# Kernel tuning notes

Hardware: AMD Instinct MI355X
Metric: run time of the kernel (lower is better)

Reference implementation:

```python
import math
import jax, jax.numpy as jnp
import numpy as np

NUM_BUCKETS = 32
MAX_DISTANCE = 128
N_HEADS = 16
D_KV = 64


def _relative_position_bucket(relative_position, num_buckets=NUM_BUCKETS, max_distance=MAX_DISTANCE):
    # bidirectional variant (encoder): half the buckets for each sign
    nb = num_buckets // 2
    n = -relative_position
    ret = (n < 0).astype(jnp.int32) * nb
    n = jnp.abs(n)
    max_exact = nb // 2
    is_small = n < max_exact
    val_if_large = max_exact + (
        jnp.log(jnp.maximum(n, 1).astype(jnp.float32) / max_exact)
        / math.log(max_distance / max_exact)
        * (nb - max_exact)
    ).astype(jnp.int32)
    val_if_large = jnp.minimum(val_if_large, nb - 1)
    return ret + jnp.where(is_small, n, val_if_large)


def setup_inputs() -> dict:
    key = jax.random.key(0)
    ks = jax.random.split(key, 6)
    d_model = 1024
    inner = N_HEADS * D_KV
    scale = 1.0 / math.sqrt(d_model)
    x = jax.random.normal(ks[0], (2, 2048, d_model), dtype=jnp.float32)
    wq = jax.random.normal(ks[1], (d_model, inner), dtype=jnp.float32) * scale
    wk = jax.random.normal(ks[2], (d_model, inner), dtype=jnp.float32) * scale
    wv = jax.random.normal(ks[3], (d_model, inner), dtype=jnp.float32) * scale
    wo = jax.random.normal(ks[4], (inner, d_model), dtype=jnp.float32) * scale
    rel_emb = jax.random.normal(ks[5], (NUM_BUCKETS, N_HEADS), dtype=jnp.float32)
    return {"x": x, "wq": wq, "wk": wk, "wv": wv, "wo": wo, "rel_emb": rel_emb}


def reference(x, wq, wk, wv, wo, rel_emb):
    B, S, D = x.shape
    # QKV projections (no bias, T5 style), split heads -> [B, S, H, Dk]
    q = (x @ wq).reshape(B, S, N_HEADS, D_KV)
    k = (x @ wk).reshape(B, S, N_HEADS, D_KV)
    v = (x @ wv).reshape(B, S, N_HEADS, D_KV)
    # NOTE: T5 does NOT scale by 1/sqrt(d_kv)
    scores = jnp.einsum("bqhd,bkhd->bhqk", q, k)  # [B, H, S, S]
    # relative position bias
    ctx = jnp.arange(S)[:, None]
    mem = jnp.arange(S)[None, :]
    buckets = _relative_position_bucket(mem - ctx)  # [S, S]
    bias = rel_emb[buckets]  # [S, S, H]
    bias = jnp.transpose(bias, (2, 0, 1))[None]  # [1, H, S, S]
    scores = scores + bias
    weights = jax.nn.softmax(scores.astype(jnp.float32), axis=-1).astype(scores.dtype)
    context = jnp.einsum("bhqk,bkhd->bqhd", weights, v).reshape(B, S, N_HEADS * D_KV)
    return context @ wo
```

## Files before the change

kernel.cpp:

```cpp
#include <hip/hip_runtime.h>
#include <hip/hip_bf16.h>

typedef __attribute__((ext_vector_type(8))) _Float16 f16x8;
typedef __attribute__((ext_vector_type(4))) float f32x4;
typedef unsigned short u16;
typedef unsigned int u32;

#define S_LEN 2048
#define NH    16
#define DK    64
#define DMODEL 1024
#define LSTR  40
#define LOG2E 1.44269504f
#define NTILES (S_LEN / 64)

union F16U { _Float16 h; u16 u; };
__device__ __forceinline__ u16 f2h(float f) {
    F16U v; v.h = (_Float16)f; return v.u;
}

__device__ __forceinline__ void gl16(const u16* g, u16* l) {
    __builtin_amdgcn_global_load_lds(
        (__attribute__((address_space(1))) void*)(u16*)g,
        (__attribute__((address_space(3))) void*)l, 16, 0, 0);
}

__global__ __launch_bounds__(256) void bias_table_kernel(
    const float* __restrict__ rel_emb, float* __restrict__ tab)
{
    int idx = blockIdx.x * 256 + threadIdx.x;
    int h = idx >> 12;
    int t = idx & 4095;
    int rp = t - 2048;
    int n = -rp;
    int ret = 0;
    if (n < 0) { ret = 16; n = -n; }
    int inner;
    if (n < 8) {
        inner = n;
    } else {
        inner = 8 + (n >= 12) + (n >= 16) + (n >= 23) + (n >= 32)
                  + (n >= 46) + (n >= 64) + (n >= 91);
        if (inner > 15) inner = 15;
    }
    tab[h * 4096 + t] = rel_emb[(ret + inner) * NH + h] * LOG2E;
}

__global__ __launch_bounds__(256) void convert_x(
    const float* __restrict__ X, u16* __restrict__ Xf)
{
    long i8 = ((long)blockIdx.x * 256 + threadIdx.x) * 8;
    float4 a = *(const float4*)&X[i8];
    float4 b = *(const float4*)&X[i8 + 4];
    *(ushort4*)&Xf[i8] =
        make_ushort4(f2h(a.x), f2h(a.y), f2h(a.z), f2h(a.w));
    *(ushort4*)&Xf[i8 + 4] =
        make_ushort4(f2h(b.x), f2h(b.y), f2h(b.z), f2h(b.w));
}

__global__ __launch_bounds__(256) void convert_wT(
    const float* __restrict__ Wq, const float* __restrict__ Wk,
    const float* __restrict__ Wv, const float* __restrict__ Wo,
    u16* __restrict__ WT)
{
    const float* src = (blockIdx.z == 0) ? Wq : (blockIdx.z == 1) ? Wk
                     : (blockIdx.z == 2) ? Wv : Wo;
    u16* dT = WT + (long)blockIdx.z * 1048576;
    __shared__ __align__(16) float T[64 * 68];
    const int k0 = blockIdx.y * 64, n0 = blockIdx.x * 64;
    const int tid = threadIdx.x;
    #pragma unroll
    for (int u = 0; u < 4; u++) {
        int w = tid + u * 256;
        int r = w >> 4, c4 = (w & 15) * 4;
        *(float4*)&T[r * 68 + c4] =
            *(const float4*)&src[(long)(k0 + r) * DMODEL + n0 + c4];
    }
    __syncthreads();
    #pragma unroll
    for (int u = 0; u < 4; u++) {
        int w = tid + u * 256;
        int n = w >> 4, kc = (w & 15) * 4;
        *(ushort4*)&dT[(long)(n0 + n) * DMODEL + k0 + kc] = make_ushort4(
            f2h(T[(kc + 0) * 68 + n]), f2h(T[(kc + 1) * 68 + n]),
            f2h(T[(kc + 2) * 68 + n]), f2h(T[(kc + 3) * 68 + n]));
    }
}

__global__ __launch_bounds__(256, 3) void gemm_qkv_mfma(
    const u16* __restrict__ Xf, const u16* __restrict__ WT,
    u16* __restrict__ Qf, u16* __restrict__ Kf, u16* __restrict__ VT)
{
    const int z = blockIdx.z;
    const u16* BT = WT + (long)z * 1048576;

    __shared__ __align__(16) u16 Ah[128 * LSTR], Bh[128 * LSTR];

    const int tid = threadIdx.x;
    const int wv = tid >> 6, lane = tid & 63;
    const int g = lane >> 4, li = lane & 15;
    const int wr = wv >> 1, wc = wv & 1;
    const int bm = blockIdx.y * 128, bn = blockIdx.x * 128;

    const int srow = tid >> 2, sq8 = (tid & 3) * 8;
    const u16* As0 = &Xf[(long)(bm + srow) * DMODEL + sq8];
    const u16* As1 = As0 + 64 * DMODEL;
    const u16* Bs0 = &BT[(long)(bn + srow) * DMODEL + sq8];
    const u16* Bs1 = Bs0 + 64 * DMODEL;
    u16* AL0 = &Ah[srow * LSTR + sq8];
    u16* AL1 = &Ah[(srow + 64) * LSTR + sq8];
    u16* BL0 = &Bh[srow * LSTR + sq8];
    u16* BL1 = &Bh[(srow + 64) * LSTR + sq8];

    f32x4 acc[4][4];
    #pragma unroll
    for (int i = 0; i < 4; i++)
        #pragma unroll
        for (int j = 0; j < 4; j++) acc[i][j] = (f32x4){0.f, 0.f, 0.f, 0.f};

    *(uint4*)AL0 = *(const uint4*)As0;
    *(uint4*)AL1 = *(const uint4*)As1;
    *(uint4*)BL0 = *(const uint4*)Bs0;
    *(uint4*)BL1 = *(const uint4*)Bs1;
    __syncthreads();

    for (int k0 = 0; k0 < DMODEL; k0 += 32) {
        const bool have = (k0 + 32) < DMODEL;
        uint4 na0, na1, nb0, nb1;
        if (have) {
            na0 = *(const uint4*)(As0 + k0 + 32);
            na1 = *(const uint4*)(As1 + k0 + 32);
            nb0 = *(const uint4*)(Bs0 + k0 + 32);
            nb1 = *(const uint4*)(Bs1 + k0 + 32);
        }

        f16x8 a_h[4], b_h[4];
        #pragma unroll
        for (int i = 0; i < 4; i++)
            a_h[i] = *(const f16x8*)&Ah[(wr * 64 + i * 16 + li) * LSTR + g * 8];
        #pragma unroll
        for (int j = 0; j < 4; j++)
            b_h[j] = *(const f16x8*)&Bh[(wc * 64 + j * 16 + li) * LSTR + g * 8];
        #pragma unroll
        for (int i = 0; i < 4; i++)
            #pragma unroll
            for (int j = 0; j < 4; j++)
                acc[i][j] = __builtin_amdgcn_mfma_f32_16x16x32_f16(
                    a_h[i], b_h[j], acc[i][j], 0, 0, 0);

        if (have) {
            __syncthreads();
            *(uint4*)AL0 = na0; *(uint4*)AL1 = na1;
            *(uint4*)BL0 = nb0; *(uint4*)BL1 = nb1;
            __syncthreads();
        }
    }

    if (z == 2) {
        #pragma unroll
        for (int i = 0; i < 4; i++) {
            int s_base = bm + wr * 64 + i * 16 + g * 4;
            int bb = s_base >> 11, s = s_base & 2047;
            #pragma unroll
            for (int j = 0; j < 4; j++) {
                int gcol = bn + wc * 64 + j * 16 + li;
                int hh = gcol >> 6, d = gcol & 63;
                long idx = (((long)(bb * NH + hh)) * DK + d) * S_LEN + s;
                *(ushort4*)&VT[idx] = make_ushort4(
                    f2h(acc[i][j][0]), f2h(acc[i][j][1]),
                    f2h(acc[i][j][2]), f2h(acc[i][j][3]));
            }
        }
    } else {
        u16* O = (z == 0) ? Qf : Kf;
        #pragma unroll
        for (int i = 0; i < 4; i++) {
            #pragma unroll
            for (int r = 0; r < 4; r++) {
                int grow = bm + wr * 64 + i * 16 + g * 4 + r;
                int bb = grow >> 11, s = grow & 2047;
                #pragma unroll
                for (int j = 0; j < 4; j++) {
                    int gcol = bn + wc * 64 + j * 16 + li;
                    int hh = gcol >> 6, d = gcol & 63;
                    long idx = (((long)(bb * NH + hh)) * S_LEN + s) * DK + d;
                    O[idx] = f2h(acc[i][j][r]);
                }
            }
        }
    }
}

__global__ __launch_bounds__(256, 3) void gemm_out_mfma(
    const u16* __restrict__ Ab, const u16* __restrict__ WT,
    float* __restrict__ O)
{
    const u16* BT = WT + 3L * 1048576;
    __shared__ __align__(16) u16 Ah[128 * LSTR], Bh[128 * LSTR];

    const int tid = threadIdx.x;
    const int wv = tid >> 6, lane = tid & 63;
    const int g = lane >> 4, li = lane & 15;
    const int wr = wv >> 1, wc = wv & 1;
    const int bm = blockIdx.y * 128, bn = blockIdx.x * 128;

    const int srow = tid >> 2, sq8 = (tid & 3) * 8;
    const u16* As0 = &Ab[(long)(bm + srow) * DMODEL + sq8];
    const u16* As1 = As0 + 64 * DMODEL;
    const u16* Bs0 = &BT[(long)(bn + srow) * DMODEL + sq8];
    const u16* Bs1 = Bs0 + 64 * DMODEL;
    u16* AL0 = &Ah[srow * LSTR + sq8];
    u16* AL1 = &Ah[(srow + 64) * LSTR + sq8];
    u16* BL0 = &Bh[srow * LSTR + sq8];
    u16* BL1 = &Bh[(srow + 64) * LSTR + sq8];

    f32x4 acc[4][4];
    #pragma unroll
    for (int i = 0; i < 4; i++)
        #pragma unroll
        for (int j = 0; j < 4; j++) acc[i][j] = (f32x4){0.f, 0.f, 0.f, 0.f};

    *(uint4*)AL0 = *(const uint4*)As0;
    *(uint4*)AL1 = *(const uint4*)As1;
    *(uint4*)BL0 = *(const uint4*)Bs0;
    *(uint4*)BL1 = *(const uint4*)Bs1;
    __syncthreads();

    for (int k0 = 0; k0 < DMODEL; k0 += 32) {
        const bool have = (k0 + 32) < DMODEL;
        uint4 na0, na1, nb0, nb1;
        if (have) {
            na0 = *(const uint4*)(As0 + k0 + 32);
            na1 = *(const uint4*)(As1 + k0 + 32);
            nb0 = *(const uint4*)(Bs0 + k0 + 32);
            nb1 = *(const uint4*)(Bs1 + k0 + 32);
        }

        f16x8 a_h[4], b_h[4];
        #pragma unroll
        for (int i = 0; i < 4; i++)
            a_h[i] = *(const f16x8*)&Ah[(wr * 64 + i * 16 + li) * LSTR + g * 8];
        #pragma unroll
        for (int j = 0; j < 4; j++)
            b_h[j] = *(const f16x8*)&Bh[(wc * 64 + j * 16 + li) * LSTR + g * 8];
        #pragma unroll
        for (int i = 0; i < 4; i++)
            #pragma unroll
            for (int j = 0; j < 4; j++)
                acc[i][j] = __builtin_amdgcn_mfma_f32_16x16x32_f16(
                    a_h[i], b_h[j], acc[i][j], 0, 0, 0);

        if (have) {
            __syncthreads();
            *(uint4*)AL0 = na0; *(uint4*)AL1 = na1;
            *(uint4*)BL0 = nb0; *(uint4*)BL1 = nb1;
            __syncthreads();
        }
    }

    #pragma unroll
    for (int i = 0; i < 4; i++)
        #pragma unroll
        for (int r = 0; r < 4; r++) {
            int grow = bm + wr * 64 + i * 16 + g * 4 + r;
            #pragma unroll
            for (int j = 0; j < 4; j++) {
                int gcol = bn + wc * 64 + j * 16 + li;
                O[(long)grow * DMODEL + gcol] = acc[i][j][r];
            }
        }
}

__global__ __launch_bounds__(256, 4) void attn_mfma(
    const u16* __restrict__ Qf, const u16* __restrict__ Kf,
    const u16* __restrict__ VT, const float* __restrict__ tab,
    u16* __restrict__ ctxb)
{
    __shared__ __align__(16) u16 Ks[2][4096];
    __shared__ __align__(16) u16 Vs[2][4096];

    const int tid = threadIdx.x;
    const int wv = tid >> 6, lane = tid & 63;
    const int g = lane >> 4, li = lane & 15;

    const int nbid = (blockIdx.x & 7) * 128 + (blockIdx.x >> 3);
    const int qblk = nbid & 31;
    const int h = (nbid >> 5) & 15;
    const int b = nbid >> 9;
    const int q0 = qblk * 64;
    const long bh = b * NH + h;
    const int qloc = wv * 16 + li;

    const u16* KhG = Kf + bh * (S_LEN * DK);
    const u16* VtG = VT + bh * (DK * S_LEN);
    const float* th0 = tab + h * 4096;
    const float* thq = th0 + 2048 - q0 - qloc + g * 4;

    const int sr  = lane >> 3;
    const int sd8 = ((lane & 7) ^ sr) * 8;
    const int c0 = wv * 2, c1 = wv * 2 + 1;
    const u16* Kg0 = KhG + (long)(c0 * 8 + sr) * DK + sd8;
    const u16* Kg1 = KhG + (long)(c1 * 8 + sr) * DK + sd8;
    const u16* Vg0 = VtG + (long)(c0 * 8 + sr) * S_LEN + sd8;
    const u16* Vg1 = VtG + (long)(c1 * 8 + sr) * S_LEN + sd8;

    const int sw  = (li & 7) * 8;
    const int roA = (g * 8) ^ sw;
    const int roB = (g * 8 + 32) ^ sw;
    const int rrow = li * 64;

    f16x8 q0f, q1f;
    {
        long qrow = bh * S_LEN + q0 + qloc;
        const u16* ph = Qf + qrow * DK + g * 8;
        q0f = *(const f16x8*)ph;  q1f = *(const f16x8*)(ph + 32);
    }
    const float bias_hi = th0[2048 + 512];
    const float bias_lo = th0[2048 - 512];

    gl16(Kg0, &Ks[0][c0 * 512]);
    gl16(Kg1, &Ks[0][c1 * 512]);
    gl16(Vg0, &Vs[0][c0 * 512]);
    gl16(Vg1, &Vs[0][c1 * 512]);
    __syncthreads();

    f32x4 Oc[4];
    #pragma unroll
    for (int n = 0; n < 4; n++) Oc[n] = (f32x4){0.f, 0.f, 0.f, 0.f};
    float mP = -1e30f, lR = 0.f;

    int cur = 0;
    for (int t = 0; t < NTILES; ++t) {
        const int kt0 = t * 64;

        if (t + 1 < NTILES) {
            const long ko = (long)(kt0 + 64) * DK;
            gl16(Kg0 + ko, &Ks[cur ^ 1][c0 * 512]);
            gl16(Kg1 + ko, &Ks[cur ^ 1][c1 * 512]);
            gl16(Vg0 + kt0 + 64, &Vs[cur ^ 1][c0 * 512]);
            gl16(Vg1 + kt0 + 64, &Vs[cur ^ 1][c1 * 512]);
        }

        float bia[4][4];
        const int dd = kt0 - q0;
        if (dd >= 192 || dd <= -192) {
            const float bc = (dd > 0) ? bias_hi : bias_lo;
            #pragma unroll
            for (int m = 0; m < 4; m++)
                #pragma unroll
                for (int r = 0; r < 4; r++) bia[m][r] = bc;
        } else {
            const float* tb = thq + kt0;
            #pragma unroll
            for (int m = 0; m < 4; m++)
                #pragma unroll
                for (int r = 0; r < 4; r++) bia[m][r] = tb[m * 16 + r];
        }

        f32x4 Sa[4];
        __builtin_amdgcn_s_setprio(1);
        #pragma unroll
        for (int m = 0; m < 4; m++) {
            const u16* kp = &Ks[cur][m * 1024 + rrow];
            f16x8 k0 = *(const f16x8*)(kp + roA);
            f16x8 k1 = *(const f16x8*)(kp + roB);
            f32x4 s = (f32x4){0.f, 0.f, 0.f, 0.f};
            s = __builtin_amdgcn_mfma_f32_16x16x32_f16(k0, q0f, s, 0, 0, 0);
            s = __builtin_amdgcn_mfma_f32_16x16x32_f16(k1, q1f, s, 0, 0, 0);
            Sa[m] = s;
        }
        __builtin_amdgcn_s_setprio(0);

        #pragma unroll
        for (int m = 0; m < 4; m++)
            #pragma unroll
            for (int r = 0; r < 4; r++)
                Sa[m][r] = fmaf(Sa[m][r], LOG2E, bia[m][r]);

        float mm[4];
        #pragma unroll
        for (int m = 0; m < 4; m++)
            mm[m] = fmaxf(fmaxf(Sa[m][0], Sa[m][1]),
                          fmaxf(Sa[m][2], Sa[m][3]));
        float pm = fmaxf(fmaxf(mm[0], mm[1]), fmaxf(mm[2], mm[3]));
        pm = fmaxf(pm, __shfl_xor(pm, 16));
        pm = fmaxf(pm, __shfl_xor(pm, 32));

        if (__any(pm > mP)) {
            float mn = fmaxf(mP, pm);
            float alpha = __builtin_amdgcn_exp2f(mP - mn);
            mP = mn;
            lR *= alpha;
            float aO[4];
            #pragma unroll
            for (int r = 0; r < 4; r++) aO[r] = __shfl(alpha, g * 4 + r);
            #pragma unroll
            for (int n = 0; n < 4; n++)
                #pragma unroll
                for (int r = 0; r < 4; r++) Oc[n][r] *= aO[r];
        }

        float sm[4];
        #pragma unroll
        for (int m = 0; m < 4; m++) {
            #pragma unroll
            for (int r = 0; r < 4; r++)
                Sa[m][r] = __builtin_amdgcn_exp2f(Sa[m][r] - mP);
            sm[m] = (Sa[m][0] + Sa[m][1]) + (Sa[m][2] + Sa[m][3]);
        }
        float ls = (sm[0] + sm[1]) + (sm[2] + sm[3]);
        ls += __shfl_xor(ls, 16);
        ls += __shfl_xor(ls, 32);
        lR += ls;

        u32 y0, y1, y2, y3, y4, y5, y6, y7;
        {
            y0 = f2h(Sa[0][0]) | ((u32)f2h(Sa[0][1]) << 16);
            y1 = f2h(Sa[0][2]) | ((u32)f2h(Sa[0][3]) << 16);
            y2 = f2h(Sa[1][0]) | ((u32)f2h(Sa[1][1]) << 16);
            y3 = f2h(Sa[1][2]) | ((u32)f2h(Sa[1][3]) << 16);
            y4 = f2h(Sa[2][0]) | ((u32)f2h(Sa[2][1]) << 16);
            y5 = f2h(Sa[2][2]) | ((u32)f2h(Sa[2][3]) << 16);
            y6 = f2h(Sa[3][0]) | ((u32)f2h(Sa[3][1]) << 16);
            y7 = f2h(Sa[3][2]) | ((u32)f2h(Sa[3][3]) << 16);
        }
        {
            bool hi = (lane & 32) != 0;
            u32 s0 = hi ? y0 : y2, s1 = hi ? y1 : y3;
            u32 s4 = hi ? y4 : y6, s5 = hi ? y5 : y7;
            u32 r0 = __shfl_xor((int)s0, 32);
            u32 r1 = __shfl_xor((int)s1, 32);
            u32 r4 = __shfl_xor((int)s4, 32);
            u32 r5 = __shfl_xor((int)s5, 32);
            if (hi) { y0 = r0; y1 = r1; y4 = r4; y5 = r5; }
            else    { y2 = r0; y3 = r1; y6 = r4; y7 = r5; }
        }
        {
            bool hi = (lane & 16) != 0;
            u32 s0 = hi ? y0 : y2, s1 = hi ? y1 : y3;
            u32 s4 = hi ? y4 : y6, s5 = hi ? y5 : y7;
            u32 r0 = __shfl_xor((int)s0, 16);
            u32 r1 = __shfl_xor((int)s1, 16);
            u32 r4 = __shfl_xor((int)s4, 16);
            u32 r5 = __shfl_xor((int)s5, 16);
            if (hi) { y0 = r0; y1 = r1; y4 = r4; y5 = r5; }
            else    { y2 = r0; y3 = r1; y6 = r4; y7 = r5; }
        }
        union { uint4 u; f16x8 h; } P0, P1;
        P0.u = make_uint4(y0, y1, y2, y3);
        P1.u = make_uint4(y4, y5, y6, y7);

        __builtin_amdgcn_s_setprio(1);
        #pragma unroll
        for (int n = 0; n < 4; n++) {
            const u16* vp = &Vs[cur][n * 1024 + rrow];
            f16x8 v0 = *(const f16x8*)(vp + roA);
            f16x8 v1 = *(const f16x8*)(vp + roB);
            Oc[n] = __builtin_amdgcn_mfma_f32_16x16x32_f16(P0.h, v0, Oc[n], 0, 0, 0);
            Oc[n] = __builtin_amdgcn_mfma_f32_16x16x32_f16(P1.h, v1, Oc[n], 0, 0, 0);
        }
        __builtin_amdgcn_s_setprio(0);

        __syncthreads();
        cur ^= 1;
    }

    float linv = 1.0f / lR;
    float iv[4];
    #pragma unroll
    for (int r = 0; r < 4; r++) iv[r] = __shfl(linv, g * 4 + r);
    #pragma unroll
    for (int n = 0; n < 4; n++)
        #pragma unroll
        for (int r = 0; r < 4; r++)
            ctxb[((long)(b * S_LEN + q0 + wv * 16 + g * 4 + r)) * DMODEL
                 + h * DK + n * 16 + li] = f2h(Oc[n][r] * iv[r]);
}

extern "C" void kernel_launch(void* const* d_in, const int* in_sizes, int n_in,
                              void* d_out, int out_size, void* d_ws, size_t ws_size,
                              hipStream_t stream)
{
    const float* x    = (const float*)d_in[0];
    const float* wq   = (const float*)d_in[1];
    const float* wk   = (const float*)d_in[2];
    const float* wv   = (const float*)d_in[3];
    const float* wo   = (const float*)d_in[4];
    const float* rel  = (const float*)d_in[5];

    u16* W0 = (u16*)d_ws;
    u16* Xf  = W0;
    u16* Qf  = W0 + 4194304;
    u16* Kf  = W0 + 8388608;
    u16* VT  = W0 + 12582912;
    u16* WT  = W0 + 16777216;
    float* tab = (float*)(W0 + 20971520);
    u16* ctxb = Xf;

    bias_table_kernel<<<dim3(256), dim3(256), 0, stream>>>(rel, tab);
    convert_x<<<dim3(2048), dim3(256), 0, stream>>>(x, Xf);
    convert_wT<<<dim3(16, 16, 4), dim3(256), 0, stream>>>(wq, wk, wv, wo, WT);
    gemm_qkv_mfma<<<dim3(8, 32, 3), dim3(256), 0, stream>>>(Xf, WT, Qf, Kf, VT);
    attn_mfma<<<dim3(1024), dim3(256), 0, stream>>>(Qf, Kf, VT, tab, ctxb);
    gemm_out_mfma<<<dim3(8, 32), dim3(256), 0, stream>>>(ctxb, WT, (float*)d_out);
}
```

Measured before the change: 216.7 us.

## Merge prep kernels and stage GEMM tiles via direct global-to-LDS loads with XOR swizzle

Fuses the bias-table, x conversion and weight transpose kernels into one launch to cut launch overhead. Both projection GEMMs now stage 128x64 tiles straight into LDS with global_load_lds, using an XOR-swizzled layout instead of the padded stride, and take a K step of 64 with two MFMA sub-steps. This removes the register round-trip and halves the number of barrier pairs. In exchange the register prefetch that overlapped loads with compute is gone, so each tile load now stalls at the barrier.

```diff
diff --git a/kernel.cpp b/kernel.cpp
--- a/kernel.cpp
+++ b/kernel.cpp
@@ -10,7 +10,6 @@
 #define NH    16
 #define DK    64
 #define DMODEL 1024
-#define LSTR  40
 #define LOG2E 1.44269504f
 #define NTILES (S_LEN / 64)
 
@@ -25,65 +24,65 @@
         (__attribute__((address_space(3))) void*)l, 16, 0, 0);
 }
 
-__global__ __launch_bounds__(256) void bias_table_kernel(
-    const float* __restrict__ rel_emb, float* __restrict__ tab)
-{
-    int idx = blockIdx.x * 256 + threadIdx.x;
-    int h = idx >> 12;
-    int t = idx & 4095;
-    int rp = t - 2048;
-    int n = -rp;
-    int ret = 0;
-    if (n < 0) { ret = 16; n = -n; }
-    int inner;
-    if (n < 8) {
-        inner = n;
-    } else {
-        inner = 8 + (n >= 12) + (n >= 16) + (n >= 23) + (n >= 32)
-                  + (n >= 46) + (n >= 64) + (n >= 91);
-        if (inner > 15) inner = 15;
-    }
-    tab[h * 4096 + t] = rel_emb[(ret + inner) * NH + h] * LOG2E;
-}
-
-__global__ __launch_bounds__(256) void convert_x(
-    const float* __restrict__ X, u16* __restrict__ Xf)
-{
-    long i8 = ((long)blockIdx.x * 256 + threadIdx.x) * 8;
-    float4 a = *(const float4*)&X[i8];
-    float4 b = *(const float4*)&X[i8 + 4];
-    *(ushort4*)&Xf[i8] =
-        make_ushort4(f2h(a.x), f2h(a.y), f2h(a.z), f2h(a.w));
-    *(ushort4*)&Xf[i8 + 4] =
-        make_ushort4(f2h(b.x), f2h(b.y), f2h(b.z), f2h(b.w));
-}
-
-__global__ __launch_bounds__(256) void convert_wT(
+__global__ __launch_bounds__(256) void prep_kernel(
+    const float* __restrict__ X,
     const float* __restrict__ Wq, const float* __restrict__ Wk,
     const float* __restrict__ Wv, const float* __restrict__ Wo,
-    u16* __restrict__ WT)
+    const float* __restrict__ rel_emb,
+    u16* __restrict__ Xf, u16* __restrict__ WT, float* __restrict__ tab)
 {
-    const float* src = (blockIdx.z == 0) ? Wq : (blockIdx.z == 1) ? Wk
-                     : (blockIdx.z == 2) ? Wv : Wo;
-    u16* dT = WT + (long)blockIdx.z * 1048576;
     __shared__ __align__(16) float T[64 * 68];
-    const int k0 = blockIdx.y * 64, n0 = blockIdx.x * 64;
+    const int bid = blockIdx.x;
     const int tid = threadIdx.x;
-    #pragma unroll
-    for (int u = 0; u < 4; u++) {
-        int w = tid + u * 256;
-        int r = w >> 4, c4 = (w & 15) * 4;
-        *(float4*)&T[r * 68 + c4] =
-            *(const float4*)&src[(long)(k0 + r) * DMODEL + n0 + c4];
-    }
-    __syncthreads();
-    #pragma unroll
-    for (int u = 0; u < 4; u++) {
-        int w = tid + u * 256;
-        int n = w >> 4, kc = (w & 15) * 4;
-        *(ushort4*)&dT[(long)(n0 + n) * DMODEL + k0 + kc] = make_ushort4(
-            f2h(T[(kc + 0) * 68 + n]), f2h(T[(kc + 1) * 68 + n]),
-            f2h(T[(kc + 2) * 68 + n]), f2h(T[(kc + 3) * 68 + n]));
+
+    if (bid < 2048) {
+        long i8 = ((long)bid * 256 + tid) * 8;
+        float4 a = *(const float4*)&X[i8];
+        float4 b = *(const float4*)&X[i8 + 4];
+        *(ushort4*)&Xf[i8] =
+            make_ushort4(f2h(a.x), f2h(a.y), f2h(a.z), f2h(a.w));
+        *(ushort4*)&Xf[i8 + 4] =
+            make_ushort4(f2h(b.x), f2h(b.y), f2h(b.z), f2h(b.w));
+    } else if (bid < 3072) {
+        const int w0 = bid - 2048;
+        const int z = w0 >> 8, rem = w0 & 255;
+        const int k0 = (rem >> 4) * 64, n0 = (rem & 15) * 64;
+        const float* src = (z == 0) ? Wq : (z == 1) ? Wk
+                         : (z == 2) ? Wv : Wo;
+        u16* dT = WT + (long)z * 1048576;
+        #pragma unroll
+        for (int u = 0; u < 4; u++) {
+            int w = tid + u * 256;
+            int r = w >> 4, c4 = (w & 15) * 4;
+            *(float4*)&T[r * 68 + c4] =
+                *(const float4*)&src[(long)(k0 + r) * DMODEL + n0 + c4];
+        }
+        __syncthreads();
+        #pragma unroll
+        for (int u = 0; u < 4; u++) {
+            int w = tid + u * 256;
+            int n = w >> 4, kc = (w & 15) * 4;
+            *(ushort4*)&dT[(long)(n0 + n) * DMODEL + k0 + kc] = make_ushort4(
+                f2h(T[(kc + 0) * 68 + n]), f2h(T[(kc + 1) * 68 + n]),
+                f2h(T[(kc + 2) * 68 + n]), f2h(T[(kc + 3) * 68 + n]));
+        }
+    } else {
+        int idx = (bid - 3072) * 256 + tid;
+        int h = idx >> 12;
+        int t = idx & 4095;
+        int rp = t - 2048;
+        int n = -rp;
+        int ret = 0;
+        if (n < 0) { ret = 16; n = -n; }
+        int inner;
+        if (n < 8) {
+            inner = n;
+        } else {
+            inner = 8 + (n >= 12) + (n >= 16) + (n >= 23) + (n >= 32)
+                      + (n >= 46) + (n >= 64) + (n >= 91);
+            if (inner > 15) inner = 15;
+        }
+        tab[h * 4096 + t] = rel_emb[(ret + inner) * NH + h] * LOG2E;
     }
 }
 
@@ -94,7 +93,7 @@
     const int z = blockIdx.z;
     const u16* BT = WT + (long)z * 1048576;
 
-    __shared__ __align__(16) u16 Ah[128 * LSTR], Bh[128 * LSTR];
+    __shared__ __align__(16) u16 Ah[128 * 64], Bh[128 * 64];
 
     const int tid = threadIdx.x;
     const int wv = tid >> 6, lane = tid & 63;
@@ -102,15 +101,30 @@
     const int wr = wv >> 1, wc = wv & 1;
     const int bm = blockIdx.y * 128, bn = blockIdx.x * 128;
 
-    const int srow = tid >> 2, sq8 = (tid & 3) * 8;
-    const u16* As0 = &Xf[(long)(bm + srow) * DMODEL + sq8];
-    const u16* As1 = As0 + 64 * DMODEL;
-    const u16* Bs0 = &BT[(long)(bn + srow) * DMODEL + sq8];
-    const u16* Bs1 = Bs0 + 64 * DMODEL;
-    u16* AL0 = &Ah[srow * LSTR + sq8];
-    u16* AL1 = &Ah[(srow + 64) * LSTR + sq8];
-    u16* BL0 = &Bh[srow * LSTR + sq8];
-    u16* BL1 = &Bh[(srow + 64) * LSTR + sq8];
+    const int sr = lane >> 3;
+    const int sb = ((lane & 7) ^ sr) * 8;
+    const u16* Asrc[4]; const u16* Bsrc[4];
+    u16* Adst[4]; u16* Bdst[4];
+    #pragma unroll
+    for (int u = 0; u < 4; u++) {
+        const int c = wv * 4 + u;
+        const int row = c * 8 + sr;
+        Asrc[u] = &Xf[(long)(bm + row) * DMODEL + sb];
+        Bsrc[u] = &BT[(long)(bn + row) * DMODEL + sb];
+        Adst[u] = &Ah[c * 512];
+        Bdst[u] = &Bh[c * 512];
+    }
+
+    int roA[4][2], roB[4][2];
+    #pragma unroll
+    for (int i = 0; i < 4; i++)
+        #pragma unroll
+        for (int ks = 0; ks < 2; ks++) {
+            int RA = wr * 64 + i * 16 + li;
+            int RB = wc * 64 + i * 16 + li;
+            roA[i][ks] = RA * 64 + (((ks * 4 + g) ^ (li & 7)) * 8);
+            roB[i][ks] = RB * 64 + (((ks * 4 + g) ^ (li & 7)) * 8);
+        }
 
     f32x4 acc[4][4];
     #pragma unroll
@@ -118,42 +132,29 @@
         #pragma unroll
         for (int j = 0; j < 4; j++) acc[i][j] = (f32x4){0.f, 0.f, 0.f, 0.f};
 
-    *(uint4*)AL0 = *(const uint4*)As0;
-    *(uint4*)AL1 = *(const uint4*)As1;
-    *(uint4*)BL0 = *(const uint4*)Bs0;
-    *(uint4*)BL1 = *(const uint4*)Bs1;
-    __syncthreads();
-
-    for (int k0 = 0; k0 < DMODEL; k0 += 32) {
-        const bool have = (k0 + 32) < DMODEL;
-        uint4 na0, na1, nb0, nb1;
-        if (have) {
-            na0 = *(const uint4*)(As0 + k0 + 32);
-            na1 = *(const uint4*)(As1 + k0 + 32);
-            nb0 = *(const uint4*)(Bs0 + k0 + 32);
-            nb1 = *(const uint4*)(Bs1 + k0 + 32);
-        }
-
-        f16x8 a_h[4], b_h[4];
-        #pragma unroll
-        for (int i = 0; i < 4; i++)
-            a_h[i] = *(const f16x8*)&Ah[(wr * 64 + i * 16 + li) * LSTR + g * 8];
-        #pragma unroll
-        for (int j = 0; j < 4; j++)
-            b_h[j] = *(const f16x8*)&Bh[(wc * 64 + j * 16 + li) * LSTR + g * 8];
-        #pragma unroll
-        for (int i = 0; i < 4; i++)
-            #pragma unroll
-            for (int j = 0; j < 4; j++)
-                acc[i][j] = __builtin_amdgcn_mfma_f32_16x16x32_f16(
-                    a_h[i], b_h[j], acc[i][j], 0, 0, 0);
-
-        if (have) {
-            __syncthreads();
-            *(uint4*)AL0 = na0; *(uint4*)AL1 = na1;
-            *(uint4*)BL0 = nb0; *(uint4*)BL1 = nb1;
-            __syncthreads();
-        }
+    for (int k0 = 0; k0 < DMODEL; k0 += 64) {
+        #pragma unroll
+        for (int u = 0; u < 4; u++) {
+            gl16(Asrc[u] + k0, Adst[u]);
+            gl16(Bsrc[u] + k0, Bdst[u]);
+        }
+        __syncthreads();
+
+        #pragma unroll
+        for (int ks = 0; ks < 2; ks++) {
+            f16x8 a_h[4], b_h[4];
+            #pragma unroll
+            for (int i = 0; i < 4; i++) a_h[i] = *(const f16x8*)&Ah[roA[i][ks]];
+            #pragma unroll
+            for (int j = 0; j < 4; j++) b_h[j] = *(const f16x8*)&Bh[roB[j][ks]];
+            #pragma unroll
+            for (int i = 0; i < 4; i++)
+                #pragma unroll
+                for (int j = 0; j < 4; j++)
+                    acc[i][j] = __builtin_amdgcn_mfma_f32_16x16x32_f16(
+                        a_h[i], b_h[j], acc[i][j], 0, 0, 0);
+        }
+        __syncthreads();
     }
 
     if (z == 2) {
@@ -196,7 +197,7 @@
     float* __restrict__ O)
 {
     const u16* BT = WT + 3L * 1048576;
-    __shared__ __align__(16) u16 Ah[128 * LSTR], Bh[128 * LSTR];
+    __shared__ __align__(16) u16 Ah[128 * 64], Bh[128 * 64];
 
     const int tid = threadIdx.x;
     const int wv = tid >> 6, lane = tid & 63;
@@ -204,15 +205,30 @@
     const int wr = wv >> 1, wc = wv & 1;
     const int bm = blockIdx.y * 128, bn = blockIdx.x * 128;
 
-    const int srow = tid >> 2, sq8 = (tid & 3) * 8;
-    const u16* As0 = &Ab[(long)(bm + srow) * DMODEL + sq8];
-    const u16* As1 = As0 + 64 * DMODEL;
-    const u16* Bs0 = &BT[(long)(bn + srow) * DMODEL + sq8];
-    const u16* Bs1 = Bs0 + 64 * DMODEL;
-    u16* AL0 = &Ah[srow * LSTR + sq8];
-    u16* AL1 = &Ah[(srow + 64) * LSTR + sq8];
-    u16* BL0 = &Bh[srow * LSTR + sq8];
-    u16* BL1 = &Bh[(srow + 64) * LSTR + sq8];
+    const int sr = lane >> 3;
+    const int sb = ((lane & 7) ^ sr) * 8;
+    const u16* Asrc[4]; const u16* Bsrc[4];
+    u16* Adst[4]; u16* Bdst[4];
+    #pragma unroll
+    for (int u = 0; u < 4; u++) {
+        const int c = wv * 4 + u;
+        const int row = c * 8 + sr;
+        Asrc[u] = &Ab[(long)(bm + row) * DMODEL + sb];
+        Bsrc[u] = &BT[(long)(bn + row) * DMODEL + sb];
+        Adst[u] = &Ah[c * 512];
+        Bdst[u] = &Bh[c * 512];
+    }
+
+    int roA[4][2], roB[4][2];
+    #pragma unroll
+    for (int i = 0; i < 4; i++)
+        #pragma unroll
+        for (int ks = 0; ks < 2; ks++) {
+            int RA = wr * 64 + i * 16 + li;
+            int RB = wc * 64 + i * 16 + li;
+            roA[i][ks] = RA * 64 + (((ks * 4 + g) ^ (li & 7)) * 8);
+            roB[i][ks] = RB * 64 + (((ks * 4 + g) ^ (li & 7)) * 8);
+        }
 
     f32x4 acc[4][4];
     #pragma unroll
@@ -220,42 +236,29 @@
         #pragma unroll
         for (int j = 0; j < 4; j++) acc[i][j] = (f32x4){0.f, 0.f, 0.f, 0.f};
 
-    *(uint4*)AL0 = *(const uint4*)As0;
-    *(uint4*)AL1 = *(const uint4*)As1;
-    *(uint4*)BL0 = *(const uint4*)Bs0;
-    *(uint4*)BL1 = *(const uint4*)Bs1;
-    __syncthreads();
-
-    for (int k0 = 0; k0 < DMODEL; k0 += 32) {
-        const bool have = (k0 + 32) < DMODEL;
-        uint4 na0, na1, nb0, nb1;
-        if (have) {
-            na0 = *(const uint4*)(As0 + k0 + 32);
-            na1 = *(const uint4*)(As1 + k0 + 32);
-            nb0 = *(const uint4*)(Bs0 + k0 + 32);
-            nb1 = *(const uint4*)(Bs1 + k0 + 32);
-        }
-
-        f16x8 a_h[4], b_h[4];
-        #pragma unroll
-        for (int i = 0; i < 4; i++)
-            a_h[i] = *(const f16x8*)&Ah[(wr * 64 + i * 16 + li) * LSTR + g * 8];
-        #pragma unroll
-        for (int j = 0; j < 4; j++)
-            b_h[j] = *(const f16x8*)&Bh[(wc * 64 + j * 16 + li) * LSTR + g * 8];
-        #pragma unroll
-        for (int i = 0; i < 4; i++)
-            #pragma unroll
-            for (int j = 0; j < 4; j++)
-                acc[i][j] = __builtin_amdgcn_mfma_f32_16x16x32_f16(
-                    a_h[i], b_h[j], acc[i][j], 0, 0, 0);
-
-        if (have) {
-            __syncthreads();
-            *(uint4*)AL0 = na0; *(uint4*)AL1 = na1;
-            *(uint4*)BL0 = nb0; *(uint4*)BL1 = nb1;
-            __syncthreads();
-        }
+    for (int k0 = 0; k0 < DMODEL; k0 += 64) {
+        #pragma unroll
+        for (int u = 0; u < 4; u++) {
+            gl16(Asrc[u] + k0, Adst[u]);
+            gl16(Bsrc[u] + k0, Bdst[u]);
+        }
+        __syncthreads();
+
+        #pragma unroll
+        for (int ks = 0; ks < 2; ks++) {
+            f16x8 a_h[4], b_h[4];
+            #pragma unroll
+            for (int i = 0; i < 4; i++) a_h[i] = *(const f16x8*)&Ah[roA[i][ks]];
+            #pragma unroll
+            for (int j = 0; j < 4; j++) b_h[j] = *(const f16x8*)&Bh[roB[j][ks]];
+            #pragma unroll
+            for (int i = 0; i < 4; i++)
+                #pragma unroll
+                for (int j = 0; j < 4; j++)
+                    acc[i][j] = __builtin_amdgcn_mfma_f32_16x16x32_f16(
+                        a_h[i], b_h[j], acc[i][j], 0, 0, 0);
+        }
+        __syncthreads();
     }
 
     #pragma unroll
@@ -497,9 +500,8 @@
     float* tab = (float*)(W0 + 20971520);
     u16* ctxb = Xf;
 
-    bias_table_kernel<<<dim3(256), dim3(256), 0, stream>>>(rel, tab);
-    convert_x<<<dim3(2048), dim3(256), 0, stream>>>(x, Xf);
-    convert_wT<<<dim3(16, 16, 4), dim3(256), 0, stream>>>(wq, wk, wv, wo, WT);
+    prep_kernel<<<dim3(3328), dim3(256), 0, stream>>>(
+        x, wq, wk, wv, wo, rel, Xf, WT, tab);
     gemm_qkv_mfma<<<dim3(8, 32, 3), dim3(256), 0, stream>>>(Xf, WT, Qf, Kf, VT);
     attn_mfma<<<dim3(1024), dim3(256), 0, stream>>>(Qf, Kf, VT, tab, ctxb);
     gemm_out_mfma<<<dim3(8, 32), dim3(256), 0, stream>>>(ctxb, WT, (float*)d_out);
```

Result: faster. 203.9 us (-5.9%).
